# Optimization experiments

Measured on AMD Instinct MI355X. Metric: run time of the kernel, lower is better.

## Reference

```python
import jax, jax.numpy as jnp
import numpy as np

# bin widths (seconds) -> integer ms, exactly as int(np.round(bin_width*1000)) in the original
BIN_SIZES_MS = [int(b) for b in np.round(np.logspace(-3.0, 0.0, 20) * 1000.0).astype(np.int64)]
SYNC_COST = 10.0
EPS = 1e-7

N_TRIALS, T_MS, N_NEURONS = 8, 2500, 16000
N_SAMPLES, K_MAX = 50, 160


def setup_inputs() -> dict:
    key = jax.random.key(0)
    k_sp, k_exp = jax.random.split(key, 2)
    spikes = (jax.random.uniform(k_sp, (N_TRIALS, T_MS, N_NEURONS)) < 0.02).astype(jnp.float32)
    rng = np.random.default_rng(42)
    sample_trials = jnp.asarray(rng.integers(0, N_TRIALS, size=N_SAMPLES), jnp.int32)
    # padded neuron-index samples drawn from (shuffled) excitatory ids
    sample_idx = jnp.asarray(rng.integers(0, N_NEURONS, size=(N_SAMPLES, K_MAX)), jnp.int32)
    # sample_counts ~ N(70, 30) clipped to [15, K_MAX], as in original (area='v1')
    counts = np.clip(rng.normal(70.0, 30.0, size=N_SAMPLES).astype(np.int32), 15, K_MAX)
    sample_counts = jnp.asarray(counts, jnp.int32)
    exp_fanos = jax.random.uniform(k_exp, (len(BIN_SIZES_MS),), minval=0.5, maxval=2.0, dtype=jnp.float32)
    return {
        "spikes": spikes,
        "exp_fanos": exp_fanos,
        "sample_trials": sample_trials,
        "sample_idx": sample_idx,
        "sample_counts": sample_counts,
    }


def _pop_fano(sel):
    # sel: [S, T] summed spike trains; conv1d(ones, stride=bin) VALID == non-overlapping binned sums
    S, T = sel.shape
    fanos = []
    for bs in BIN_SIZES_MS:
        nb = T // bs
        counts = sel[:, : nb * bs].reshape(S, nb, bs).sum(axis=-1)  # [S, nb]
        mean_c = jnp.maximum(counts.mean(axis=1), EPS)
        var_c = counts.var(axis=1)  # population variance, matches tf.math.reduce_variance
        fanos.append(jnp.mean(var_c / mean_c))
    return jnp.stack(fanos)


def reference(spikes, exp_fanos, sample_trials, sample_idx, sample_counts):
    S, K = sample_idx.shape
    T = spikes.shape[1]
    mask = (jnp.arange(K)[None, :] < sample_counts[:, None]).astype(spikes.dtype)  # [S, K]
    # gather spikes[trial_i, :, idx_ij] -> [S, T, K] (avoids materializing [S, T, N])
    gathered = spikes[sample_trials[:, None, None],
                      jnp.arange(T)[None, :, None],
                      sample_idx[:, None, :]]
    sel = jnp.einsum('stk,sk->st', gathered, mask)  # masked sum over sampled neurons
    fanos = _pop_fano(sel)
    return SYNC_COST * jnp.mean(jnp.square(exp_fanos - fanos))
```

## Files before the change

kernel.cpp:

```cpp
#include <hip/hip_runtime.h>

#define N_TRIALS  8
#define T_MS      2500
#define N_NEURONS 16000
#define N_SAMPLES 50
#define K_MAX     160
#define N_BINS    20
#define SYNC_COST 10.0f
#define EPS_F     1e-7f

__device__ const int BIN_SIZES[N_BINS] = {1, 1, 2, 3, 4, 6, 9, 13, 18, 26,
                                          38, 55, 78, 113, 162, 234, 336, 483, 695, 1000};

__global__ __launch_bounds__(256) void sel_kernel(
    const float* __restrict__ spikes,
    const int*   __restrict__ trials,
    const int*   __restrict__ idx,
    const int*   __restrict__ counts,
    float*       __restrict__ sel)
{
    const int s      = blockIdx.x;
    const int t_base = blockIdx.y * 100;
    const int tid    = threadIdx.x;
    const int lane   = tid & 63;
    const int wave   = tid >> 6;

    __shared__ int sidx[K_MAX];
    if (tid < K_MAX) sidx[tid] = idx[s * K_MAX + tid];
    __syncthreads();

    const int cnt   = counts[s];
    const int trial = trials[s];
    const float* base = spikes + (size_t)trial * T_MS * N_NEURONS;

    for (int tt = wave; tt < 100; tt += 4) {
        const int t = t_base + tt;
        const float* row = base + (size_t)t * N_NEURONS;
        float acc = 0.f;
        for (int k = lane; k < cnt; k += 64) {
            acc += row[sidx[k]];
        }
        #pragma unroll
        for (int off = 32; off > 0; off >>= 1)
            acc += __shfl_down(acc, off, 64);
        if (lane == 0) sel[s * T_MS + t] = acc;
    }
}

__global__ __launch_bounds__(256) void fano_kernel(
    const float* __restrict__ sel,
    float*       __restrict__ term)
{
    const int s   = blockIdx.x;
    const int b   = blockIdx.y;
    const int bs  = BIN_SIZES[b];
    const int nb  = T_MS / bs;
    const int tid = threadIdx.x;
    const float* srow = sel + s * T_MS;

    __shared__ float red[256];
    __shared__ float s_mean;

    float psum = 0.f;
    for (int j = tid; j < nb; j += 256) {
        const float* p = srow + j * bs;
        float c = 0.f;
        for (int u = 0; u < bs; ++u) c += p[u];
        psum += c;
    }
    red[tid] = psum;
    __syncthreads();
    for (int off = 128; off > 0; off >>= 1) {
        if (tid < off) red[tid] += red[tid + off];
        __syncthreads();
    }
    if (tid == 0) s_mean = red[0] / (float)nb;
    __syncthreads();
    const float mean = s_mean;

    float pvar = 0.f;
    for (int j = tid; j < nb; j += 256) {
        const float* p = srow + j * bs;
        float c = 0.f;
        for (int u = 0; u < bs; ++u) c += p[u];
        const float d = c - mean;
        pvar += d * d;
    }
    red[tid] = pvar;
    __syncthreads();
    for (int off = 128; off > 0; off >>= 1) {
        if (tid < off) red[tid] += red[tid + off];
        __syncthreads();
    }
    if (tid == 0) {
        const float var = red[0] / (float)nb;
        const float m = mean > EPS_F ? mean : EPS_F;
        term[b * N_SAMPLES + s] = var / m;
    }
}

__global__ void loss_kernel(
    const float* __restrict__ term,
    const float* __restrict__ exp_fanos,
    float*       __restrict__ out)
{
    const int tid = threadIdx.x;
    __shared__ float sq[N_BINS];
    if (tid < N_BINS) {
        float sum = 0.f;
        for (int s = 0; s < N_SAMPLES; ++s) sum += term[tid * N_SAMPLES + s];
        const float fano = sum / (float)N_SAMPLES;
        const float d = exp_fanos[tid] - fano;
        sq[tid] = d * d;
    }
    __syncthreads();
    if (tid == 0) {
        float tot = 0.f;
        for (int b = 0; b < N_BINS; ++b) tot += sq[b];
        out[0] = SYNC_COST * tot / (float)N_BINS;
    }
}

extern "C" void kernel_launch(void* const* d_in, const int* in_sizes, int n_in,
                              void* d_out, int out_size, void* d_ws, size_t ws_size,
                              hipStream_t stream)
{
    const float* spikes    = (const float*)d_in[0];
    const float* exp_fanos = (const float*)d_in[1];
    const int*   trials    = (const int*)d_in[2];
    const int*   idx       = (const int*)d_in[3];
    const int*   counts    = (const int*)d_in[4];
    float*       out       = (float*)d_out;

    float* sel  = (float*)d_ws;
    float* term = sel + N_SAMPLES * T_MS;

    sel_kernel<<<dim3(N_SAMPLES, 25), 256, 0, stream>>>(spikes, trials, idx, counts, sel);
    fano_kernel<<<dim3(N_SAMPLES, N_BINS), 256, 0, stream>>>(sel, term);
    loss_kernel<<<1, 64, 0, stream>>>(term, exp_fanos, out);
}
```

Baseline: 1.652 ms.

## Group samples by trial so one block gathers all samples per time chunk

Adds a prep kernel that buckets sample ids by trial. The gather kernel is re-gridded over (time chunk, trial) and stages every sample's column list for that trial in shared memory. Each wave then walks a spike row for all samples sharing the trial, so rows touched by several samples get reused through the cache instead of being fetched by separate blocks. This costs an extra launch, a serial prefix sum, and uneven block work, since some trials have no samples.

```diff
diff --git a/kernel.cpp b/kernel.cpp
--- a/kernel.cpp
+++ b/kernel.cpp
@@ -8,42 +8,82 @@
 #define N_BINS    20
 #define SYNC_COST 10.0f
 #define EPS_F     1e-7f
+#define T_CHUNK   20
 
 __device__ const int BIN_SIZES[N_BINS] = {1, 1, 2, 3, 4, 6, 9, 13, 18, 26,
                                           38, 55, 78, 113, 162, 234, 336, 483, 695, 1000};
 
+__global__ void prep_kernel(const int* __restrict__ trials,
+                            int* __restrict__ tm_ns,
+                            int* __restrict__ tm_samp)
+{
+    const int tr = threadIdx.x;
+    if (tr < N_TRIALS) {
+        int n = 0;
+        for (int s = 0; s < N_SAMPLES; ++s)
+            if (trials[s] == tr) tm_samp[tr * N_SAMPLES + n++] = s;
+        tm_ns[tr] = n;
+    }
+}
+
 __global__ __launch_bounds__(256) void sel_kernel(
     const float* __restrict__ spikes,
-    const int*   __restrict__ trials,
     const int*   __restrict__ idx,
     const int*   __restrict__ counts,
+    const int*   __restrict__ tm_ns,
+    const int*   __restrict__ tm_samp,
     float*       __restrict__ sel)
 {
-    const int s      = blockIdx.x;
-    const int t_base = blockIdx.y * 100;
-    const int tid    = threadIdx.x;
-    const int lane   = tid & 63;
-    const int wave   = tid >> 6;
+    const int tr   = blockIdx.y;
+    const int t0   = blockIdx.x * T_CHUNK;
+    const int tid  = threadIdx.x;
+    const int lane = tid & 63;
+    const int wave = tid >> 6;
 
-    __shared__ int sidx[K_MAX];
-    if (tid < K_MAX) sidx[tid] = idx[s * K_MAX + tid];
+    __shared__ int s_ns;
+    __shared__ int s_sid[N_SAMPLES];
+    __shared__ int s_cnt[N_SAMPLES];
+    __shared__ int s_off[N_SAMPLES + 1];
+    __shared__ int s_cols[N_SAMPLES * K_MAX];
+
+    if (tid == 0) s_ns = tm_ns[tr];
+    __syncthreads();
+    const int ns = s_ns;
+    if (ns == 0) return;
+
+    if (tid < ns) {
+        const int sid = tm_samp[tr * N_SAMPLES + tid];
+        s_sid[tid] = sid;
+        s_cnt[tid] = counts[sid];
+    }
+    __syncthreads();
+    if (tid == 0) {
+        int off = 0;
+        for (int j = 0; j < ns; ++j) { s_off[j] = off; off += s_cnt[j]; }
+        s_off[ns] = off;
+    }
+    __syncthreads();
+    for (int j = 0; j < ns; ++j) {
+        const int cnt = s_cnt[j], sid = s_sid[j], off = s_off[j];
+        for (int k = tid; k < cnt; k += 256)
+            s_cols[off + k] = idx[sid * K_MAX + k];
+    }
     __syncthreads();
 
-    const int cnt   = counts[s];
-    const int trial = trials[s];
-    const float* base = spikes + (size_t)trial * T_MS * N_NEURONS;
-
-    for (int tt = wave; tt < 100; tt += 4) {
-        const int t = t_base + tt;
-        const float* row = base + (size_t)t * N_NEURONS;
-        float acc = 0.f;
-        for (int k = lane; k < cnt; k += 64) {
-            acc += row[sidx[k]];
+    const float* tb = spikes + (size_t)tr * T_MS * N_NEURONS;
+    for (int tt = wave; tt < T_CHUNK; tt += 4) {
+        const int t = t0 + tt;
+        const float* row = tb + (size_t)t * N_NEURONS;
+        for (int j = 0; j < ns; ++j) {
+            const int cnt = s_cnt[j], off = s_off[j];
+            float acc = 0.f;
+            for (int k = lane; k < cnt; k += 64)
+                acc += row[s_cols[off + k]];
+            #pragma unroll
+            for (int o = 32; o > 0; o >>= 1)
+                acc += __shfl_down(acc, o, 64);
+            if (lane == 0) sel[s_sid[j] * T_MS + t] = acc;
         }
-        #pragma unroll
-        for (int off = 32; off > 0; off >>= 1)
-            acc += __shfl_down(acc, off, 64);
-        if (lane == 0) sel[s * T_MS + t] = acc;
     }
 }
 
@@ -132,10 +172,14 @@
     const int*   counts    = (const int*)d_in[4];
     float*       out       = (float*)d_out;
 
-    float* sel  = (float*)d_ws;
-    float* term = sel + N_SAMPLES * T_MS;
+    float* sel   = (float*)d_ws;
+    float* term  = sel + N_SAMPLES * T_MS;
+    int*   tm_ns = (int*)(term + N_BINS * N_SAMPLES);
+    int*   tm_sa = tm_ns + N_TRIALS;
 
-    sel_kernel<<<dim3(N_SAMPLES, 25), 256, 0, stream>>>(spikes, trials, idx, counts, sel);
+    prep_kernel<<<1, 64, 0, stream>>>(trials, tm_ns, tm_sa);
+    sel_kernel<<<dim3(T_MS / T_CHUNK, N_TRIALS), 256, 0, stream>>>(
+        spikes, idx, counts, tm_ns, tm_sa, sel);
     fano_kernel<<<dim3(N_SAMPLES, N_BINS), 256, 0, stream>>>(sel, term);
     loss_kernel<<<1, 64, 0, stream>>>(term, exp_fanos, out);
 }
```

After: 1.634 ms. No clear change (-1.1%).
